# Kernel optimization log

Hardware: AMD Instinct MI355X
Metric: run time of the kernel (lower is better)

The kernel has to match this reference:

```python
import jax, jax.numpy as jnp
import numpy as np

B, S, DIN, DOUT = 2, 2048, 4096, 4096


def setup_inputs() -> dict:
    key = jax.random.key(0)
    k1, k2, k3, k4 = jax.random.split(key, 4)
    x = jax.random.normal(k1, (B, S, DIN), dtype=jnp.float32)
    # int8 quantized weight buffer, values in [-128, 127] as in torch.randint(-2**7, 2**7, ...)
    weight = jax.random.randint(k2, (DOUT, DIN), -128, 128, dtype=jnp.int32).astype(jnp.int8)
    scale = jax.random.normal(k3, (DOUT,), dtype=jnp.float32)
    bias = jax.random.normal(k4, (1, DOUT), dtype=jnp.float32)
    return {"x": x, "weight": weight, "scale": scale, "bias": bias}


def reference(x, weight, scale, bias):
    # F.linear(x, weight.to(x.dtype)) * scale + bias
    w = weight.astype(x.dtype)                      # [DOUT, DIN]
    out = jnp.einsum('bsi,oi->bso', x, w)           # [B, S, DOUT]
    out = out * scale                               # per-output-channel dequant scale
    out = out + bias                                # broadcast [1, DOUT]
    return out
```

## Files before the change

### kernel.cpp

```cpp
#include <hip/hip_runtime.h>
#include <hip/hip_bf16.h>
#include <stdint.h>

#define M_DIM 4096
#define N_DIM 4096
#define K_DIM 4096

#define BM 128
#define BN 128
#define BK 64
#define KT_TILES (K_DIM / BK)
#define TILE_ELEMS (BM * BK)
#define TILE_BYTES (TILE_ELEMS * 2)

typedef unsigned short u16;
typedef __attribute__((ext_vector_type(8))) __bf16 bf16x8;
typedef __attribute__((ext_vector_type(4))) float f32x4;


__device__ __forceinline__ uint32_t pack_bf16_rn(float a, float b) {
  uint32_t ua = (__float_as_uint(a) + 0x8000u) >> 16;
  uint32_t ub = (__float_as_uint(b) + 0x8000u) & 0xffff0000u;
  return ua | ub;
}

__device__ __forceinline__ uint32_t pack_bf16_int(int a, int b) {
  uint32_t ha = __float_as_uint((float)a) >> 16;
  uint32_t hb = __float_as_uint((float)b) & 0xffff0000u;
  return ha | hb;
}

__device__ __forceinline__ void gload16(const void* g, void* l) {
  __builtin_amdgcn_global_load_lds(
      (__attribute__((address_space(1))) void*)(uintptr_t)g,
      (__attribute__((address_space(3))) void*)l,
      16, 0, 0);
}


__global__ __launch_bounds__(256) void convert_x_kernel(
    const float* __restrict__ x, u16* __restrict__ wsA) {
  uint32_t tid = blockIdx.x * 256u + threadIdx.x;
  uint32_t c  = tid & 7u;
  uint32_t r  = (tid >> 3) & 127u;
  uint32_t kt = (tid >> 10) & 63u;
  uint32_t mt = tid >> 16;

  const float* src = x + (((size_t)(mt * 128u + r)) << 12) + (kt << 6) + (c << 3);
  float4 f0 = *(const float4*)src;
  float4 f1 = *(const float4*)(src + 4);

  uint4 o;
  o.x = pack_bf16_rn(f0.x, f0.y);
  o.y = pack_bf16_rn(f0.z, f0.w);
  o.z = pack_bf16_rn(f1.x, f1.y);
  o.w = pack_bf16_rn(f1.z, f1.w);

  uint32_t dst_chunk = ((mt * 64u + kt) << 10) + (r << 3) + (c ^ (r & 7u));
  *(uint4*)(wsA + ((size_t)dst_chunk << 3)) = o;
}

__global__ __launch_bounds__(256) void convert_w_kernel(
    const int* __restrict__ w, u16* __restrict__ wsB) {
  uint32_t tid = blockIdx.x * 256u + threadIdx.x;
  uint32_t c  = tid & 7u;
  uint32_t r  = (tid >> 3) & 127u;
  uint32_t kt = (tid >> 10) & 63u;
  uint32_t nt = tid >> 16;

  const int* src = w + (((size_t)(nt * 128u + r)) << 12) + (kt << 6) + (c << 3);
  int4 i0 = *(const int4*)src;
  int4 i1 = *(const int4*)(src + 4);

  uint4 o;
  o.x = pack_bf16_int(i0.x, i0.y);
  o.y = pack_bf16_int(i0.z, i0.w);
  o.z = pack_bf16_int(i1.x, i1.y);
  o.w = pack_bf16_int(i1.z, i1.w);

  uint32_t dst_chunk = ((nt * 64u + kt) << 10) + (r << 3) + (c ^ (r & 7u));
  *(uint4*)(wsB + ((size_t)dst_chunk << 3)) = o;
}


__global__ __launch_bounds__(256, 3) void gemm_kernel(
    const u16* __restrict__ wsA, const u16* __restrict__ wsB,
    const float* __restrict__ scale, const float* __restrict__ bias,
    float* __restrict__ out) {
  __shared__ __attribute__((aligned(16))) u16 ldsA[TILE_ELEMS];
  __shared__ __attribute__((aligned(16))) u16 ldsB[TILE_ELEMS];

  const int tid   = threadIdx.x;
  const int lane  = tid & 63;
  const int wid   = tid >> 6;
  const int wr    = wid >> 1;
  const int wc    = wid & 1;
  const int nt    = blockIdx.x;
  const int mt    = blockIdx.y;
  const int r16   = lane & 15;
  const int khalf = lane >> 4;

  f32x4 acc[4][4];
#pragma unroll
  for (int m = 0; m < 4; ++m)
#pragma unroll
    for (int n = 0; n < 4; ++n)
      acc[m][n] = (f32x4){0.f, 0.f, 0.f, 0.f};

  const char* gA = (const char*)(wsA + (size_t)mt * KT_TILES * TILE_ELEMS);
  const char* gB = (const char*)(wsB + (size_t)nt * KT_TILES * TILE_ELEMS);

  int aoff[4], boff[4];
#pragma unroll
  for (int m = 0; m < 4; ++m) {
    int rowa = (wr << 6) + (m << 4) + r16;
    aoff[m] = (rowa << 7) + (((khalf ^ (rowa & 7)) & 7) << 4);
    int rowb = (wc << 6) + (m << 4) + r16;
    boff[m] = (rowb << 7) + (((khalf ^ (rowb & 7)) & 7) << 4);
  }

  for (int kt = 0; kt < KT_TILES; ++kt) {
    __syncthreads();
    const char* srcA = gA + (size_t)kt * TILE_BYTES;
    const char* srcB = gB + (size_t)kt * TILE_BYTES;
#pragma unroll
    for (int r = 0; r < 4; ++r) {
      int o = (r << 12) + (wid << 10);
      gload16(srcA + o + lane * 16, (char*)ldsA + o);
      gload16(srcB + o + lane * 16, (char*)ldsB + o);
    }
    __syncthreads();

    bf16x8 a0[4], b0[4], a1[4], b1[4];
#pragma unroll
    for (int m = 0; m < 4; ++m) {
      a0[m] = *(const bf16x8*)((const char*)ldsA + aoff[m]);
      a1[m] = *(const bf16x8*)((const char*)ldsA + (aoff[m] ^ 64));
      b0[m] = *(const bf16x8*)((const char*)ldsB + boff[m]);
      b1[m] = *(const bf16x8*)((const char*)ldsB + (boff[m] ^ 64));
    }
#pragma unroll
    for (int m = 0; m < 4; ++m)
#pragma unroll
      for (int n = 0; n < 4; ++n)
        acc[m][n] = __builtin_amdgcn_mfma_f32_16x16x32_bf16(a0[m], b0[n], acc[m][n], 0, 0, 0);
#pragma unroll
    for (int m = 0; m < 4; ++m)
#pragma unroll
      for (int n = 0; n < 4; ++n)
        acc[m][n] = __builtin_amdgcn_mfma_f32_16x16x32_bf16(a1[m], b1[n], acc[m][n], 0, 0, 0);
  }

#pragma unroll
  for (int n = 0; n < 4; ++n) {
    int col = (nt << 7) + (wc << 6) + (n << 4) + r16;
    float s  = scale[col];
    float bb = bias[col];
#pragma unroll
    for (int m = 0; m < 4; ++m) {
      int row0 = (mt << 7) + (wr << 6) + (m << 4) + (khalf << 2);
#pragma unroll
      for (int j = 0; j < 4; ++j) {
        out[((size_t)(row0 + j) << 12) + col] = acc[m][n][j] * s + bb;
      }
    }
  }
}

__global__ __launch_bounds__(256) void fallback_kernel(
    const float* __restrict__ x, const int* __restrict__ w,
    const float* __restrict__ scale, const float* __restrict__ bias,
    float* __restrict__ out) {
  size_t t = (size_t)blockIdx.x * 256 + threadIdx.x;
  if (t >= (size_t)M_DIM * N_DIM) return;
  int col = (int)(t & (N_DIM - 1));
  int row = (int)(t >> 12);
  const float* xr = x + ((size_t)row << 12);
  const int* wr = w + ((size_t)col << 12);
  float acc = 0.f;
  for (int k = 0; k < K_DIM; k += 4) {
    float4 xv = *(const float4*)(xr + k);
    int4 wv = *(const int4*)(wr + k);
    acc += xv.x * (float)wv.x;
    acc += xv.y * (float)wv.y;
    acc += xv.z * (float)wv.z;
    acc += xv.w * (float)wv.w;
  }
  out[t] = acc * scale[col] + bias[col];
}

extern "C" void kernel_launch(void* const* d_in, const int* in_sizes, int n_in,
                              void* d_out, int out_size, void* d_ws, size_t ws_size,
                              hipStream_t stream) {
  const float* x     = (const float*)d_in[0];
  const int*   w     = (const int*)d_in[1];
  const float* scale = (const float*)d_in[2];
  const float* bias  = (const float*)d_in[3];
  float*       out   = (float*)d_out;

  if (ws_size >= (size_t)64 * 1024 * 1024) {
    u16* wsA = (u16*)d_ws;
    u16* wsB = wsA + (size_t)M_DIM * K_DIM;

    convert_x_kernel<<<8192, 256, 0, stream>>>(x, wsA);
    convert_w_kernel<<<8192, 256, 0, stream>>>(w, wsB);

    dim3 grid(N_DIM / BN, M_DIM / BM);
    gemm_kernel<<<grid, 256, 0, stream>>>(wsA, wsB, scale, bias, out);
  } else {
    fallback_kernel<<<(M_DIM * (size_t)N_DIM + 255) / 256, 256, 0, stream>>>(
        x, w, scale, bias, out);
  }
}
```

Baseline: 297.8 us.

## Use 256x256 tiles with double-buffered LDS pipeline and fused conversion

The GEMM moves from 128x128 tiles with 4 waves to 256x256 tiles with 8 waves. Global-to-LDS loads are double-buffered across 128KB of shared memory, with staged waitcnt/barrier phases interleaved with MFMA groups, raised wave priority around the MFMAs, and a block-index swizzle for L2 locality. The two conversion kernels are merged into one launch, writing the new 256-row tile layout. The aim is to hide load latency and raise data reuse per tile. The cost is more register pressure, lower occupancy, and fragile hand-counted vmcnt synchronisation.

Measured after the change: 272.4 us. -8.5%, faster.

```diff
diff --git a/kernel.cpp b/kernel.cpp
--- a/kernel.cpp
+++ b/kernel.cpp
@@ -5,13 +5,6 @@
 #define M_DIM 4096
 #define N_DIM 4096
 #define K_DIM 4096
-
-#define BM 128
-#define BN 128
-#define BK 64
-#define KT_TILES (K_DIM / BK)
-#define TILE_ELEMS (BM * BK)
-#define TILE_BYTES (TILE_ELEMS * 2)
 
 typedef unsigned short u16;
 typedef __attribute__((ext_vector_type(8))) __bf16 bf16x8;
@@ -37,134 +30,209 @@
       16, 0, 0);
 }
 
-
-__global__ __launch_bounds__(256) void convert_x_kernel(
-    const float* __restrict__ x, u16* __restrict__ wsA) {
-  uint32_t tid = blockIdx.x * 256u + threadIdx.x;
+__global__ __launch_bounds__(256) void convert_kernel(
+    const float* __restrict__ x, const int* __restrict__ w,
+    u16* __restrict__ wsA, u16* __restrict__ wsB) {
+  uint32_t bid = blockIdx.x;
+  bool isA = bid < 8192;
+  uint32_t tid = (isA ? bid : (bid - 8192)) * 256u + threadIdx.x;
   uint32_t c  = tid & 7u;
   uint32_t r  = (tid >> 3) & 127u;
-  uint32_t kt = (tid >> 10) & 63u;
-  uint32_t mt = tid >> 16;
-
-  const float* src = x + (((size_t)(mt * 128u + r)) << 12) + (kt << 6) + (c << 3);
-  float4 f0 = *(const float4*)src;
-  float4 f1 = *(const float4*)(src + 4);
+  uint32_t h  = (tid >> 10) & 1u;
+  uint32_t kt = (tid >> 11) & 63u;
+  uint32_t st = tid >> 17;
+
+  uint32_t row = st * 256u + h * 128u + r;
+  uint32_t col = kt * 64u + c * 8u;
+  size_t dst16 = ((size_t)(st * 64u + kt) << 11)
+               + (h << 10) + (r << 3) + (c ^ (r & 7u));
 
   uint4 o;
-  o.x = pack_bf16_rn(f0.x, f0.y);
-  o.y = pack_bf16_rn(f0.z, f0.w);
-  o.z = pack_bf16_rn(f1.x, f1.y);
-  o.w = pack_bf16_rn(f1.z, f1.w);
-
-  uint32_t dst_chunk = ((mt * 64u + kt) << 10) + (r << 3) + (c ^ (r & 7u));
-  *(uint4*)(wsA + ((size_t)dst_chunk << 3)) = o;
-}
-
-__global__ __launch_bounds__(256) void convert_w_kernel(
-    const int* __restrict__ w, u16* __restrict__ wsB) {
-  uint32_t tid = blockIdx.x * 256u + threadIdx.x;
-  uint32_t c  = tid & 7u;
-  uint32_t r  = (tid >> 3) & 127u;
-  uint32_t kt = (tid >> 10) & 63u;
-  uint32_t nt = tid >> 16;
-
-  const int* src = w + (((size_t)(nt * 128u + r)) << 12) + (kt << 6) + (c << 3);
-  int4 i0 = *(const int4*)src;
-  int4 i1 = *(const int4*)(src + 4);
-
-  uint4 o;
-  o.x = pack_bf16_int(i0.x, i0.y);
-  o.y = pack_bf16_int(i0.z, i0.w);
-  o.z = pack_bf16_int(i1.x, i1.y);
-  o.w = pack_bf16_int(i1.z, i1.w);
-
-  uint32_t dst_chunk = ((nt * 64u + kt) << 10) + (r << 3) + (c ^ (r & 7u));
-  *(uint4*)(wsB + ((size_t)dst_chunk << 3)) = o;
-}
-
-
-__global__ __launch_bounds__(256, 3) void gemm_kernel(
+  if (isA) {
+    const float* src = x + ((size_t)row << 12) + col;
+    float4 f0 = *(const float4*)src;
+    float4 f1 = *(const float4*)(src + 4);
+    o.x = pack_bf16_rn(f0.x, f0.y); o.y = pack_bf16_rn(f0.z, f0.w);
+    o.z = pack_bf16_rn(f1.x, f1.y); o.w = pack_bf16_rn(f1.z, f1.w);
+    *(uint4*)((char*)wsA + (dst16 << 4)) = o;
+  } else {
+    const int* src = w + ((size_t)row << 12) + col;
+    int4 i0 = *(const int4*)src;
+    int4 i1 = *(const int4*)(src + 4);
+    o.x = pack_bf16_int(i0.x, i0.y); o.y = pack_bf16_int(i0.z, i0.w);
+    o.z = pack_bf16_int(i1.x, i1.y); o.w = pack_bf16_int(i1.z, i1.w);
+    *(uint4*)((char*)wsB + (dst16 << 4)) = o;
+  }
+}
+
+__global__ __launch_bounds__(512, 2) void gemm_kernel(
     const u16* __restrict__ wsA, const u16* __restrict__ wsB,
     const float* __restrict__ scale, const float* __restrict__ bias,
     float* __restrict__ out) {
-  __shared__ __attribute__((aligned(16))) u16 ldsA[TILE_ELEMS];
-  __shared__ __attribute__((aligned(16))) u16 ldsB[TILE_ELEMS];
+  __shared__ __attribute__((aligned(16))) char smem[131072];
 
   const int tid   = threadIdx.x;
   const int lane  = tid & 63;
   const int wid   = tid >> 6;
-  const int wr    = wid >> 1;
-  const int wc    = wid & 1;
-  const int nt    = blockIdx.x;
-  const int mt    = blockIdx.y;
+  const int wr    = wid >> 2;
+  const int wc    = wid & 3;
   const int r16   = lane & 15;
   const int khalf = lane >> 4;
 
-  f32x4 acc[4][4];
-#pragma unroll
-  for (int m = 0; m < 4; ++m)
-#pragma unroll
-    for (int n = 0; n < 4; ++n)
-      acc[m][n] = (f32x4){0.f, 0.f, 0.f, 0.f};
-
-  const char* gA = (const char*)(wsA + (size_t)mt * KT_TILES * TILE_ELEMS);
-  const char* gB = (const char*)(wsB + (size_t)nt * KT_TILES * TILE_ELEMS);
-
-  int aoff[4], boff[4];
-#pragma unroll
-  for (int m = 0; m < 4; ++m) {
-    int rowa = (wr << 6) + (m << 4) + r16;
-    aoff[m] = (rowa << 7) + (((khalf ^ (rowa & 7)) & 7) << 4);
-    int rowb = (wc << 6) + (m << 4) + r16;
-    boff[m] = (rowb << 7) + (((khalf ^ (rowb & 7)) & 7) << 4);
-  }
-
-  for (int kt = 0; kt < KT_TILES; ++kt) {
-    __syncthreads();
-    const char* srcA = gA + (size_t)kt * TILE_BYTES;
-    const char* srcB = gB + (size_t)kt * TILE_BYTES;
-#pragma unroll
-    for (int r = 0; r < 4; ++r) {
-      int o = (r << 12) + (wid << 10);
-      gload16(srcA + o + lane * 16, (char*)ldsA + o);
-      gload16(srcB + o + lane * 16, (char*)ldsB + o);
+  const int bid = (int)blockIdx.x;
+  const int swz = ((bid & 7) << 5) + (bid >> 3);
+  const int mt = swz >> 4;
+  const int nt = swz & 15;
+
+  const char* gA = (const char*)wsA + ((size_t)mt << 21);
+  const char* gB = (const char*)wsB + ((size_t)nt << 21);
+
+  int aoff[4][2], boff[2][2];
+#pragma unroll
+  for (int kk = 0; kk < 2; ++kk) {
+    int ch = ((kk * 4 + khalf) ^ (r16 & 7)) << 4;
+#pragma unroll
+    for (int m = 0; m < 4; ++m)
+      aoff[m][kk] = ((wr << 6) + (m << 4) + r16) * 128 + ch;
+#pragma unroll
+    for (int n = 0; n < 2; ++n)
+      boff[n][kk] = ((wc << 5) + (n << 4) + r16) * 128 + ch;
+  }
+
+  const int su = wid << 10;
+  const int sl = su + lane * 16;
+
+#define STAGE(gbase, dstbase)                                   \
+  do {                                                          \
+    gload16((gbase) + sl,        smem + (dstbase) + su);        \
+    gload16((gbase) + sl + 8192, smem + (dstbase) + su + 8192); \
+  } while (0)
+
+  f32x4 acc[2][4][2][2];
+#pragma unroll
+  for (int mh = 0; mh < 2; ++mh)
+#pragma unroll
+    for (int m = 0; m < 4; ++m)
+#pragma unroll
+      for (int nh = 0; nh < 2; ++nh)
+#pragma unroll
+        for (int n = 0; n < 2; ++n)
+          acc[mh][m][nh][n] = (f32x4){0.f, 0.f, 0.f, 0.f};
+
+  bf16x8 af[4][2];
+  bf16x8 bfr[2][2][2];
+
+  STAGE(gA, 0);
+  STAGE(gB, 32768);
+  STAGE(gB + 16384, 49152);
+  STAGE(gA + 16384, 16384);
+
+  for (int t = 0; t < 64; ++t) {
+    const int lb = (t & 1) << 16;
+    const int sb = lb ^ 65536;
+    const int ktn = (t + 1) & 63;
+    const char* gAn = gA + ((size_t)ktn << 15);
+    const char* gBn = gB + ((size_t)ktn << 15);
+
+    asm volatile("s_waitcnt vmcnt(4)" ::: "memory");
+    __builtin_amdgcn_s_barrier();
+    asm volatile("" ::: "memory");
+    __builtin_amdgcn_sched_barrier(0);
+#pragma unroll
+    for (int m = 0; m < 4; ++m)
+#pragma unroll
+      for (int kk = 0; kk < 2; ++kk)
+        af[m][kk] = *(const bf16x8*)(smem + lb + aoff[m][kk]);
+#pragma unroll
+    for (int n = 0; n < 2; ++n)
+#pragma unroll
+      for (int kk = 0; kk < 2; ++kk)
+        bfr[0][n][kk] = *(const bf16x8*)(smem + lb + 32768 + boff[n][kk]);
+    STAGE(gAn, sb);
+    __builtin_amdgcn_s_setprio(1);
+#pragma unroll
+    for (int m = 0; m < 4; ++m)
+#pragma unroll
+      for (int n = 0; n < 2; ++n)
+#pragma unroll
+        for (int kk = 0; kk < 2; ++kk)
+          acc[0][m][0][n] = __builtin_amdgcn_mfma_f32_16x16x32_bf16(
+              af[m][kk], bfr[0][n][kk], acc[0][m][0][n], 0, 0, 0);
+    __builtin_amdgcn_s_setprio(0);
+
+    asm volatile("s_waitcnt vmcnt(4)" ::: "memory");
+    __builtin_amdgcn_s_barrier();
+    asm volatile("" ::: "memory");
+    __builtin_amdgcn_sched_barrier(0);
+#pragma unroll
+    for (int n = 0; n < 2; ++n)
+#pragma unroll
+      for (int kk = 0; kk < 2; ++kk)
+        bfr[1][n][kk] = *(const bf16x8*)(smem + lb + 49152 + boff[n][kk]);
+    STAGE(gBn, sb + 32768);
+    __builtin_amdgcn_s_setprio(1);
+#pragma unroll
+    for (int m = 0; m < 4; ++m)
+#pragma unroll
+      for (int n = 0; n < 2; ++n)
+#pragma unroll
+        for (int kk = 0; kk < 2; ++kk)
+          acc[0][m][1][n] = __builtin_amdgcn_mfma_f32_16x16x32_bf16(
+              af[m][kk], bfr[1][n][kk], acc[0][m][1][n], 0, 0, 0);
+    __builtin_amdgcn_s_setprio(0);
+
+    asm volatile("s_waitcnt vmcnt(4)" ::: "memory");
+    __builtin_amdgcn_s_barrier();
+    asm volatile("" ::: "memory");
+    __builtin_amdgcn_sched_barrier(0);
+#pragma unroll
+    for (int m = 0; m < 4; ++m)
+#pragma unroll
+      for (int kk = 0; kk < 2; ++kk)
+        af[m][kk] = *(const bf16x8*)(smem + lb + 16384 + aoff[m][kk]);
+    STAGE(gBn + 16384, sb + 49152);
+    __builtin_amdgcn_s_setprio(1);
+#pragma unroll
+    for (int m = 0; m < 4; ++m)
+#pragma unroll
+      for (int n = 0; n < 2; ++n)
+#pragma unroll
+        for (int kk = 0; kk < 2; ++kk)
+          acc[1][m][0][n] = __builtin_amdgcn_mfma_f32_16x16x32_bf16(
+              af[m][kk], bfr[0][n][kk], acc[1][m][0][n], 0, 0, 0);
+    __builtin_amdgcn_s_setprio(0);
+
+    STAGE(gAn + 16384, sb + 16384);
+    __builtin_amdgcn_s_setprio(1);
+#pragma unroll
+    for (int m = 0; m < 4; ++m)
+#pragma unroll
+      for (int n = 0; n < 2; ++n)
+#pragma unroll
+        for (int kk = 0; kk < 2; ++kk)
+          acc[1][m][1][n] = __builtin_amdgcn_mfma_f32_16x16x32_bf16(
+              af[m][kk], bfr[1][n][kk], acc[1][m][1][n], 0, 0, 0);
+    __builtin_amdgcn_s_setprio(0);
+  }
+#undef STAGE
+
+#pragma unroll
+  for (int nh = 0; nh < 2; ++nh)
+#pragma unroll
+    for (int n = 0; n < 2; ++n) {
+      const int col = (nt << 8) + (nh << 7) + (wc << 5) + (n << 4) + r16;
+      const float s  = scale[col];
+      const float bb = bias[col];
+#pragma unroll
+      for (int mh = 0; mh < 2; ++mh)
+#pragma unroll
+        for (int m = 0; m < 4; ++m) {
+          const int row0 = (mt << 8) + (mh << 7) + (wr << 6) + (m << 4) + (khalf << 2);
+#pragma unroll
+          for (int j = 0; j < 4; ++j)
+            out[((size_t)(row0 + j) << 12) + col] = acc[mh][m][nh][n][j] * s + bb;
+        }
     }
-    __syncthreads();
-
-    bf16x8 a0[4], b0[4], a1[4], b1[4];
-#pragma unroll
-    for (int m = 0; m < 4; ++m) {
-      a0[m] = *(const bf16x8*)((const char*)ldsA + aoff[m]);
-      a1[m] = *(const bf16x8*)((const char*)ldsA + (aoff[m] ^ 64));
-      b0[m] = *(const bf16x8*)((const char*)ldsB + boff[m]);
-      b1[m] = *(const bf16x8*)((const char*)ldsB + (boff[m] ^ 64));
-    }
-#pragma unroll
-    for (int m = 0; m < 4; ++m)
-#pragma unroll
-      for (int n = 0; n < 4; ++n)
-        acc[m][n] = __builtin_amdgcn_mfma_f32_16x16x32_bf16(a0[m], b0[n], acc[m][n], 0, 0, 0);
-#pragma unroll
-    for (int m = 0; m < 4; ++m)
-#pragma unroll
-      for (int n = 0; n < 4; ++n)
-        acc[m][n] = __builtin_amdgcn_mfma_f32_16x16x32_bf16(a1[m], b1[n], acc[m][n], 0, 0, 0);
-  }
-
-#pragma unroll
-  for (int n = 0; n < 4; ++n) {
-    int col = (nt << 7) + (wc << 6) + (n << 4) + r16;
-    float s  = scale[col];
-    float bb = bias[col];
-#pragma unroll
-    for (int m = 0; m < 4; ++m) {
-      int row0 = (mt << 7) + (wr << 6) + (m << 4) + (khalf << 2);
-#pragma unroll
-      for (int j = 0; j < 4; ++j) {
-        out[((size_t)(row0 + j) << 12) + col] = acc[m][n][j] * s + bb;
-      }
-    }
-  }
 }
 
 __global__ __launch_bounds__(256) void fallback_kernel(
@@ -176,11 +244,11 @@
   int col = (int)(t & (N_DIM - 1));
   int row = (int)(t >> 12);
   const float* xr = x + ((size_t)row << 12);
-  const int* wr = w + ((size_t)col << 12);
+  const int* wrow = w + ((size_t)col << 12);
   float acc = 0.f;
   for (int k = 0; k < K_DIM; k += 4) {
     float4 xv = *(const float4*)(xr + k);
-    int4 wv = *(const int4*)(wr + k);
+    int4 wv = *(const int4*)(wrow + k);
     acc += xv.x * (float)wv.x;
     acc += xv.y * (float)wv.y;
     acc += xv.z * (float)wv.z;
@@ -202,13 +270,10 @@
     u16* wsA = (u16*)d_ws;
     u16* wsB = wsA + (size_t)M_DIM * K_DIM;
 
-    convert_x_kernel<<<8192, 256, 0, stream>>>(x, wsA);
-    convert_w_kernel<<<8192, 256, 0, stream>>>(w, wsB);
-
-    dim3 grid(N_DIM / BN, M_DIM / BM);
-    gemm_kernel<<<grid, 256, 0, stream>>>(wsA, wsB, scale, bias, out);
+    convert_kernel<<<16384, 256, 0, stream>>>(x, w, wsA, wsB);
+    gemm_kernel<<<256, 512, 0, stream>>>(wsA, wsB, scale, bias, out);
   } else {
-    fallback_kernel<<<(M_DIM * (size_t)N_DIM + 255) / 256, 256, 0, stream>>>(
+    fallback_kernel<<<((size_t)M_DIM * N_DIM + 255) / 256, 256, 0, stream>>>(
         x, w, scale, bias, out);
   }
 }
```
